# Performance work log

Hardware: AMD Instinct MI355X
Metric: run time of the kernel (lower is better)

Reference implementation:

```python
import jax, jax.numpy as jnp
import numpy as np
import math

N_NODES = 50000
N_EDGES = 1600000
C = 256
H = 8
HD = C // H


def setup_inputs() -> dict:
    key = jax.random.key(0)
    ks = jax.random.split(key, 16)
    s = 0.02
    d = {
        "feat": jax.random.normal(ks[0], (N_NODES, C), jnp.float32),
        "edge_src": jax.random.randint(ks[1], (N_EDGES,), 0, N_NODES),
        "edge_dst": jax.random.randint(ks[2], (N_EDGES,), 0, N_NODES),
        # torch nn.Linear weights are [out, in]
        "Wq": jax.random.normal(ks[3], (C, C), jnp.float32) * s,
        "bq": jnp.zeros((C,), jnp.float32),
        "Wk": jax.random.normal(ks[4], (C, C), jnp.float32) * s,
        "bk": jnp.zeros((C,), jnp.float32),
        "Wv": jax.random.normal(ks[5], (C, C), jnp.float32) * s,
        "bv": jnp.zeros((C,), jnp.float32),
        "Wp": jax.random.normal(ks[6], (C, C), jnp.float32) * s,
        "bp": jnp.zeros((C,), jnp.float32),
        "ln_g": jnp.ones((C,), jnp.float32),
        "ln_b": jnp.zeros((C,), jnp.float32),
        "W1": jax.random.normal(ks[7], (4 * C, C), jnp.float32) * s,
        "b1": jnp.zeros((4 * C,), jnp.float32),
        "W2": jax.random.normal(ks[8], (C, 4 * C), jnp.float32) * s,
        "b2": jnp.zeros((C,), jnp.float32),
    }
    return d


def _layernorm(x, g, b, eps=1e-5):
    mu = jnp.mean(x, axis=-1, keepdims=True)
    var = jnp.mean(jnp.square(x - mu), axis=-1, keepdims=True)
    return (x - mu) * jax.lax.rsqrt(var + eps) * g + b


def reference(feat, edge_src, edge_dst, Wq, bq, Wk, bk, Wv, bv, Wp, bp,
              ln_g, ln_b, W1, b1, W2, b2):
    n = feat.shape[0]
    q = (feat @ Wq.T + bq).reshape(n, H, HD)
    k = (feat @ Wk.T + bk).reshape(n, H, HD)
    v = (feat @ Wv.T + bv).reshape(n, H, HD)

    # per-edge attention logits: (q[dst] * k[src]).sum(-1) / sqrt(head_dim), clamped
    score = jnp.einsum('ehd,ehd->eh', q[edge_dst], k[edge_src])  # [E, H]
    score = jnp.clip(score / math.sqrt(HD), -10.0, 10.0)

    # destination-grouped (segment) softmax over incoming edges
    smax = jax.ops.segment_max(score, edge_dst, num_segments=n)
    smax = jnp.where(jnp.isfinite(smax), smax, 0.0)  # guard empty segments
    ex = jnp.exp(score - smax[edge_dst])
    den = jax.ops.segment_sum(ex, edge_dst, num_segments=n)
    alpha = ex / den[edge_dst]  # [E, H]

    # weighted scatter-aggregate: sum_e alpha_e * v[src_e] into dst
    wv = jax.ops.segment_sum(alpha[:, :, None] * v[edge_src], edge_dst,
                             num_segments=n).reshape(n, C)

    y = wv @ Wp.T + bp
    x = feat + y
    h = _layernorm(x, ln_g, ln_b)
    h = jax.nn.gelu(h @ W1.T + b1, approximate=False) @ W2.T + b2
    return x + h
```

## Files before the change

### kernel.cpp

```cpp
#include <hip/hip_runtime.h>
#include <hip/hip_bf16.h>

#define CDIM 256
#define NH 8
#define HDIM 32

typedef short bf8 __attribute__((ext_vector_type(8)));
typedef float f32x4 __attribute__((ext_vector_type(4)));
typedef float f32x2 __attribute__((ext_vector_type(2)));

__device__ __forceinline__ float bf2f(ushort u) {
  union { unsigned int i; float f; } x; x.i = ((unsigned int)u) << 16; return x.f;
}
__device__ __forceinline__ ushort f2bf(float f) {
  union { float f; unsigned int i; } x; x.f = f;
  unsigned int lsb = (x.i >> 16) & 1u;
  unsigned int r = x.i + 0x7fffu + lsb;
  return (ushort)(r >> 16);
}

__device__ __forceinline__ float dec_e4m3_sw(unsigned int b) {
  unsigned int s = b >> 7, e = (b >> 3) & 15, m = b & 7;
  float v = (e == 0) ? (float)m * 0.001953125f
                     : (float)(8 + m) * 0.125f * exp2f((float)((int)e - 7));
  return s ? -v : v;
}
__device__ __forceinline__ unsigned char enc_e4m3_sw(float f) {
  union { float f; unsigned int u; } x; x.f = f;
  unsigned int s = (x.u >> 31) << 7;
  float a = fabsf(f);
  if (!(a > 0.f)) return (unsigned char)s;
  if (a > 448.f) a = 448.f;
  int e = 0; float mant = frexpf(a, &e);
  int E = e + 6;
  unsigned int out;
  if (E <= 0) {
    int m = (int)rintf(a * 512.f);
    out = (m > 7) ? (s | (1u << 3)) : (s | (unsigned)m);
  } else {
    int m = (int)rintf(mant * 16.f);
    if (m == 16) { m = 8; E++; }
    if (E > 15 || (E == 15 && m - 8 > 6)) { E = 15; m = 14; }
    out = s | ((unsigned)E << 3) | (unsigned)(m - 8);
  }
  return (unsigned char)out;
}
template <bool HI>
__device__ __forceinline__ f32x2 fp8x2_f32(unsigned int w) {
#if __has_builtin(__builtin_amdgcn_cvt_pk_f32_fp8)
  return __builtin_amdgcn_cvt_pk_f32_fp8(w, HI);
#else
  unsigned int b0 = HI ? ((w >> 16) & 0xffu) : (w & 0xffu);
  unsigned int b1 = HI ? (w >> 24) : ((w >> 8) & 0xffu);
  f32x2 r; r[0] = dec_e4m3_sw(b0); r[1] = dec_e4m3_sw(b1); return r;
#endif
}
__device__ __forceinline__ unsigned char f32_fp8(float f) {
#if __has_builtin(__builtin_amdgcn_cvt_pk_fp8_f32)
  return (unsigned char)(__builtin_amdgcn_cvt_pk_fp8_f32(f, f, 0, false) & 0xff);
#else
  return enc_e4m3_sw(f);
#endif
}

__device__ __forceinline__ float fast_gelu(float t) {
  float u = 0.7978845608028654f * (t + 0.044715f * t * t * t);
  float ez = __expf(2.f * u);
  float th = 1.f - 2.f * __builtin_amdgcn_rcpf(ez + 1.f);
  return 0.5f * t * (1.f + th);
}

__device__ __forceinline__ void gload_lds16(const ushort* g, ushort* l) {
  __builtin_amdgcn_global_load_lds((const __attribute__((address_space(1))) unsigned int*)g,
                                   (__attribute__((address_space(3))) unsigned int*)l,
                                   16, 0, 0);
}

__global__ void k_cast4(const float4* __restrict__ s, ushort4* __restrict__ d, int n4) {
  int i = blockIdx.x * blockDim.x + threadIdx.x;
  if (i < n4) {
    float4 v = s[i];
    ushort4 o;
    o.x = f2bf(v.x); o.y = f2bf(v.y); o.z = f2bf(v.z); o.w = f2bf(v.w);
    d[i] = o;
  }
}

__global__ void k_hist(const int* __restrict__ dst, int E, int* __restrict__ deg) {
  int i = blockIdx.x * blockDim.x + threadIdx.x;
  if (i < E) atomicAdd(&deg[dst[i]], 1);
}

__global__ __launch_bounds__(1024) void k_scan1(const int* __restrict__ deg, int N,
                                                int* __restrict__ rowptr, int* __restrict__ bsum) {
  __shared__ int s[1024];
  int t = threadIdx.x;
  int i = blockIdx.x * 1024 + t;
  int val = (i < N) ? deg[i] : 0;
  s[t] = val;
  __syncthreads();
  for (int off = 1; off < 1024; off <<= 1) {
    int add = (t >= off) ? s[t - off] : 0;
    __syncthreads();
    s[t] += add;
    __syncthreads();
  }
  if (i < N) rowptr[i + 1] = s[t];
  if (t == 1023) bsum[blockIdx.x] = s[t];
}

__global__ void k_scan2(int* __restrict__ bsum, int nb) {
  if (threadIdx.x == 0 && blockIdx.x == 0) {
    int run = 0;
    for (int j = 0; j < nb; ++j) { int t = bsum[j]; bsum[j] = run; run += t; }
  }
}

__global__ void k_scan3(int* __restrict__ rowptr, const int* __restrict__ bsum, int N) {
  int i = blockIdx.x * blockDim.x + threadIdx.x;
  if (i < N) rowptr[i + 1] += bsum[i >> 10];
  if (i == 0) rowptr[0] = 0;
}

__global__ void k_scatter(const int* __restrict__ src, const int* __restrict__ dst, int E,
                          const int* __restrict__ rowptr, int* __restrict__ cur,
                          int* __restrict__ csr_src) {
  int i = blockIdx.x * blockDim.x + threadIdx.x;
  if (i < E) {
    int d = dst[i];
    int pos = rowptr[d] + atomicAdd(&cur[d], 1);
    csr_src[pos] = src[i];
  }
}

__device__ __forceinline__ void stage_tile(const ushort* __restrict__ S, int ld,
                                           int r0, int nr, int k0,
                                           ushort* lds, int wave, int lane) {
#pragma unroll
  for (int j = 0; j < 2; ++j) {
    int g = wave * 128 + j * 64 + lane;
    int row = g >> 2, slot = g & 3;
    int rr = r0 + row; rr = (rr < nr) ? rr : (nr - 1);
    const ushort* src = S + (size_t)rr * ld + k0 + ((slot ^ (row & 3)) << 3);
    gload_lds16(src, &lds[(size_t)(wave * 128 + j * 64) * 8]);
  }
}

__device__ __forceinline__ void gemm128_core(const ushort* __restrict__ A, int lda, int rowt, int nA,
                                             const ushort* __restrict__ B, int ldb, int colt, int nB,
                                             int K, ushort* lA, ushort* lB, f32x4* acc) {
  int tid = threadIdx.x;
  int wave = tid >> 6, lane = tid & 63;
  int m = lane & 15, quad = lane >> 4;
  int r0w = (wave & 1) * 64, c0w = (wave >> 1) * 64;
  int sw = (quad ^ (m & 3)) << 3;

  for (int k0 = 0; k0 < K; k0 += 32) {
    __syncthreads();
    stage_tile(A, lda, rowt, nA, k0, lA, wave, lane);
    stage_tile(B, ldb, colt, nB, k0, lB, wave, lane);
    __syncthreads();

    bf8 a[4], b[4];
#pragma unroll
    for (int ri = 0; ri < 4; ++ri)
      a[ri] = *(const bf8*)&lA[(r0w + ri * 16 + m) * 32 + sw];
#pragma unroll
    for (int cj = 0; cj < 4; ++cj)
      b[cj] = *(const bf8*)&lB[(c0w + cj * 16 + m) * 32 + sw];
#pragma unroll
    for (int ri = 0; ri < 4; ++ri)
#pragma unroll
      for (int cj = 0; cj < 4; ++cj)
        acc[ri * 4 + cj] = __builtin_amdgcn_mfma_f32_16x16x32_bf16(a[ri], b[cj], acc[ri * 4 + cj], 0, 0, 0);
  }
}

__global__ __launch_bounds__(256) void k_qkvf(const ushort* __restrict__ featb,
                                              const ushort* __restrict__ Wqkv,
                                              const float* __restrict__ bq, const float* __restrict__ bk,
                                              const float* __restrict__ bv,
                                              ushort* __restrict__ q,
                                              unsigned char* __restrict__ k8,
                                              unsigned char* __restrict__ v8, int N) {
  __shared__ ushort lA[128 * 32];
  __shared__ ushort lB[128 * 32];
  int rowt = blockIdx.x * 128, colt = blockIdx.y * 128;
  int which = colt >> 8;
  const float* bias = (which == 0) ? bq : (which == 1) ? bk : bv;
  int tid = threadIdx.x;
  int wave = tid >> 6, lane = tid & 63, m = lane & 15, quad = lane >> 4;
  int r0w = (wave & 1) * 64, c0w = (wave >> 1) * 64;

  f32x4 acc[16];
#pragma unroll
  for (int j = 0; j < 16; ++j) acc[j] = (f32x4){0.f, 0.f, 0.f, 0.f};

  gemm128_core(featb, CDIM, rowt, N, Wqkv, CDIM, colt, 768, CDIM, lA, lB, acc);

  unsigned char* o8 = (which == 1) ? k8 : v8;
#pragma unroll
  for (int cj = 0; cj < 4; ++cj) {
    int col = (colt + c0w + cj * 16 + m) & 255;
    float bs = bias[col];
#pragma unroll
    for (int ri = 0; ri < 4; ++ri)
#pragma unroll
      for (int i = 0; i < 4; ++i) {
        int r = rowt + r0w + ri * 16 + quad * 4 + i;
        if (r < N) {
          float vv = acc[ri * 4 + cj][i] + bs;
          if (which == 0) q[(size_t)r * CDIM + col] = f2bf(vv);
          else            o8[(size_t)r * CDIM + col] = f32_fp8(vv);
        }
      }
  }
}

__global__ __launch_bounds__(256) void k_proj(const ushort* __restrict__ wv,
                                              const ushort* __restrict__ Wp,
                                              const float* __restrict__ bp,
                                              const float* __restrict__ feat,
                                              float* __restrict__ x, int N) {
  __shared__ ushort lA[128 * 32];
  __shared__ ushort lB[128 * 32];
  int rowt = blockIdx.x * 128, colt = blockIdx.y * 128;
  int tid = threadIdx.x;
  int wave = tid >> 6, lane = tid & 63, m = lane & 15, quad = lane >> 4;
  int r0w = (wave & 1) * 64, c0w = (wave >> 1) * 64;

  f32x4 acc[16];
#pragma unroll
  for (int j = 0; j < 16; ++j) acc[j] = (f32x4){0.f, 0.f, 0.f, 0.f};

  gemm128_core(wv, CDIM, rowt, N, Wp, CDIM, colt, 256, CDIM, lA, lB, acc);

#pragma unroll
  for (int cj = 0; cj < 4; ++cj) {
    int col = colt + c0w + cj * 16 + m;
    float bs = bp[col];
#pragma unroll
    for (int ri = 0; ri < 4; ++ri)
#pragma unroll
      for (int i = 0; i < 4; ++i) {
        int r = rowt + r0w + ri * 16 + quad * 4 + i;
        if (r < N)
          x[(size_t)r * CDIM + col] = acc[ri * 4 + cj][i] + bs + feat[(size_t)r * CDIM + col];
      }
  }
}

__global__ __launch_bounds__(256) void k_g1(const ushort* __restrict__ h,
                                            const ushort* __restrict__ W1c,
                                            const float* __restrict__ b1c,
                                            ushort* __restrict__ hid, int N) {
  __shared__ ushort lA[128 * 32];
  __shared__ ushort lB[128 * 32];
  int rowt = blockIdx.x * 128, colt = blockIdx.y * 128;
  int tid = threadIdx.x;
  int wave = tid >> 6, lane = tid & 63, m = lane & 15, quad = lane >> 4;
  int r0w = (wave & 1) * 64, c0w = (wave >> 1) * 64;

  f32x4 acc[16];
#pragma unroll
  for (int j = 0; j < 16; ++j) acc[j] = (f32x4){0.f, 0.f, 0.f, 0.f};

  gemm128_core(h, CDIM, rowt, N, W1c, CDIM, colt, 512, CDIM, lA, lB, acc);

#pragma unroll
  for (int cj = 0; cj < 4; ++cj) {
    int col = colt + c0w + cj * 16 + m;
    float bs = b1c[col];
#pragma unroll
    for (int ri = 0; ri < 4; ++ri)
#pragma unroll
      for (int i = 0; i < 4; ++i) {
        int r = rowt + r0w + ri * 16 + quad * 4 + i;
        if (r < N) hid[(size_t)r * 512 + col] = f2bf(fast_gelu(acc[ri * 4 + cj][i] + bs));
      }
  }
}

__global__ __launch_bounds__(256) void k_g2(const ushort* __restrict__ hid,
                                            const ushort* __restrict__ W2c,
                                            const float* __restrict__ b2,
                                            float* __restrict__ out, int N, int first) {
  __shared__ ushort lA[128 * 32];
  __shared__ ushort lB[128 * 32];
  int rowt = blockIdx.x * 128, colt = blockIdx.y * 128;
  int tid = threadIdx.x;
  int wave = tid >> 6, lane = tid & 63, m = lane & 15, quad = lane >> 4;
  int r0w = (wave & 1) * 64, c0w = (wave >> 1) * 64;

  f32x4 acc[16];
#pragma unroll
  for (int j = 0; j < 16; ++j) acc[j] = (f32x4){0.f, 0.f, 0.f, 0.f};

  gemm128_core(hid, 512, rowt, N, W2c, 1024, colt, 256, 512, lA, lB, acc);

#pragma unroll
  for (int cj = 0; cj < 4; ++cj) {
    int col = colt + c0w + cj * 16 + m;
    float bs = first ? b2[col] : 0.f;
#pragma unroll
    for (int ri = 0; ri < 4; ++ri)
#pragma unroll
      for (int i = 0; i < 4; ++i) {
        int r = rowt + r0w + ri * 16 + quad * 4 + i;
        if (r < N) {
          size_t idx = (size_t)r * CDIM + col;
          out[idx] = out[idx] + acc[ri * 4 + cj][i] + bs;
        }
      }
  }
}

__global__ __launch_bounds__(256) void k_edge_agg(const ushort* __restrict__ q,
                                                  const unsigned char* __restrict__ kk8,
                                                  const unsigned char* __restrict__ vv8,
                                                  const int* __restrict__ rowptr,
                                                  const int* __restrict__ csr_src,
                                                  int N,
                                                  ushort* __restrict__ wv) {
  int wave = threadIdx.x >> 6, lane = threadIdx.x & 63;
  int n = blockIdx.x * 4 + wave;
  if (n >= N) return;

  int el = lane >> 3, h = lane & 7;
  int beg = rowptr[n], end = rowptr[n + 1];
  int deg = end - beg;

  float qf[32];
  {
    const ushort* qp = q + (size_t)n * CDIM + h * HDIM;
#pragma unroll
    for (int g = 0; g < 4; ++g) {
      bf8 qv = *(const bf8*)(qp + g * 8);
#pragma unroll
      for (int j = 0; j < 8; ++j) qf[g * 8 + j] = bf2f((ushort)qv[j]);
    }
  }

  float accv[4] = {0.f, 0.f, 0.f, 0.f};
  float den_part = 0.f;

  for (int c0 = 0; c0 < deg; c0 += 8) {
    int src = 0;
    float e = 0.f;
    if (c0 + el < deg) {
      src = csr_src[beg + c0 + el];
      const unsigned char* kp = kk8 + (size_t)src * CDIM + h * HDIM;
      uint4 w0 = *(const uint4*)kp;
      uint4 w1 = *(const uint4*)(kp + 16);
      unsigned int ws[8] = {w0.x, w0.y, w0.z, w0.w, w1.x, w1.y, w1.z, w1.w};
      float dot = 0.f;
#pragma unroll
      for (int j = 0; j < 8; ++j) {
        f32x2 lo = fp8x2_f32<false>(ws[j]);
        f32x2 hi = fp8x2_f32<true>(ws[j]);
        dot = fmaf(qf[j * 4 + 0], lo[0], dot);
        dot = fmaf(qf[j * 4 + 1], lo[1], dot);
        dot = fmaf(qf[j * 4 + 2], hi[0], dot);
        dot = fmaf(qf[j * 4 + 3], hi[1], dot);
      }
      float s = dot * 0.17677669529663687f;
      s = fminf(10.f, fmaxf(-10.f, s));
      e = __expf(s - 10.f);
    }
    den_part += e;

#pragma unroll
    for (int j = 0; j < 8; ++j) {
      int sj = __shfl(src, j << 3);
      float ej = __shfl(e, (j << 3) | (lane >> 3));
      unsigned int vw = *(const unsigned int*)(vv8 + (size_t)sj * CDIM + lane * 4);
      f32x2 lo = fp8x2_f32<false>(vw);
      f32x2 hi = fp8x2_f32<true>(vw);
      accv[0] = fmaf(ej, lo[0], accv[0]);
      accv[1] = fmaf(ej, lo[1], accv[1]);
      accv[2] = fmaf(ej, hi[0], accv[2]);
      accv[3] = fmaf(ej, hi[1], accv[3]);
    }
  }

  float den = den_part;
  den += __shfl_xor(den, 8);
  den += __shfl_xor(den, 16);
  den += __shfl_xor(den, 32);
  float denh = __shfl(den, lane >> 3);

  float inv = (deg > 0) ? (1.f / denh) : 0.f;
  ushort4 o;
  o.x = f2bf(accv[0] * inv);
  o.y = f2bf(accv[1] * inv);
  o.z = f2bf(accv[2] * inv);
  o.w = f2bf(accv[3] * inv);
  *(ushort4*)(wv + (size_t)n * CDIM + lane * 4) = o;
}

__global__ __launch_bounds__(256) void k_ln(const float* __restrict__ x,
                                            const float* __restrict__ g,
                                            const float* __restrict__ b,
                                            ushort* __restrict__ h,
                                            float* __restrict__ out) {
  int row = blockIdx.x * 4 + (threadIdx.x >> 6);
  int lane = threadIdx.x & 63;
  const float* xr = x + (size_t)row * CDIM;
  float4 xv = *(const float4*)(xr + lane * 4);
  *(float4*)(out + (size_t)row * CDIM + lane * 4) = xv;
  float s = xv.x + xv.y + xv.z + xv.w;
  float ss = xv.x * xv.x + xv.y * xv.y + xv.z * xv.z + xv.w * xv.w;
#pragma unroll
  for (int msk = 1; msk <= 32; msk <<= 1) {
    s += __shfl_xor(s, msk);
    ss += __shfl_xor(ss, msk);
  }
  float mu = s * (1.f / CDIM);
  float var = ss * (1.f / CDIM) - mu * mu;
  float rs = rsqrtf(var + 1e-5f);
  float xe[4] = {xv.x, xv.y, xv.z, xv.w};
#pragma unroll
  for (int t = 0; t < 4; ++t) {
    int cc = lane * 4 + t;
    h[(size_t)row * CDIM + cc] = f2bf((xe[t] - mu) * rs * g[cc] + b[cc]);
  }
}

extern "C" void kernel_launch(void* const* d_in, const int* in_sizes, int n_in,
                              void* d_out, int out_size, void* d_ws, size_t ws_size,
                              hipStream_t stream) {
  const float* feat = (const float*)d_in[0];
  const int* esrc = (const int*)d_in[1];
  const int* edst = (const int*)d_in[2];
  const float* Wq = (const float*)d_in[3];
  const float* bq = (const float*)d_in[4];
  const float* Wk = (const float*)d_in[5];
  const float* bk = (const float*)d_in[6];
  const float* Wv = (const float*)d_in[7];
  const float* bv = (const float*)d_in[8];
  const float* Wp = (const float*)d_in[9];
  const float* bp = (const float*)d_in[10];
  const float* lng = (const float*)d_in[11];
  const float* lnb = (const float*)d_in[12];
  const float* W1 = (const float*)d_in[13];
  const float* b1 = (const float*)d_in[14];
  const float* W2 = (const float*)d_in[15];
  const float* b2 = (const float*)d_in[16];

  const int N = in_sizes[0] / CDIM;
  const int E = in_sizes[1];
  const size_t NC2 = (size_t)N * CDIM * 2;
  const size_t NC1 = (size_t)N * CDIM;

  char* w = (char*)d_ws;
  ushort* q   = (ushort*)(w);
  unsigned char* k8 = (unsigned char*)(w + NC2);
  unsigned char* v8 = (unsigned char*)(w + NC2 + NC1);
  ushort* wvb = (ushort*)(w + 3 * NC2);
  ushort* featb = (ushort*)(w + 3 * NC2);
  float*  x   = (float*)(w);
  ushort* h   = (ushort*)(w + 2 * NC2);
  ushort* hid = (ushort*)(w);

  char* csr = w + 4 * NC2;
  int* rowptr  = (int*)(csr);
  int* deg     = (int*)(csr + 200064);
  int* csr_src = (int*)(csr + 400128);
  int* bsum    = (int*)(csr + 400128 + (size_t)E * 4);

  char* wb = csr + 400128 + (size_t)E * 4 + 256;
  ushort* Wqb = (ushort*)(wb);
  ushort* Wkb = (ushort*)(wb + 131072);
  ushort* Wvb = (ushort*)(wb + 262144);
  ushort* Wpb = (ushort*)(wb + 393216);
  ushort* W1b = (ushort*)(wb + 524288);
  ushort* W2b = (ushort*)(wb + 1048576);

  const int nb = (N + 1023) / 1024;
  const int RT128 = (N + 127) / 128;

  k_cast4<<<(16384 + 255) / 256, 256, 0, stream>>>((const float4*)Wq, (ushort4*)Wqb, 16384);
  k_cast4<<<(16384 + 255) / 256, 256, 0, stream>>>((const float4*)Wk, (ushort4*)Wkb, 16384);
  k_cast4<<<(16384 + 255) / 256, 256, 0, stream>>>((const float4*)Wv, (ushort4*)Wvb, 16384);
  k_cast4<<<(16384 + 255) / 256, 256, 0, stream>>>((const float4*)Wp, (ushort4*)Wpb, 16384);
  k_cast4<<<(65536 + 255) / 256, 256, 0, stream>>>((const float4*)W1, (ushort4*)W1b, 65536);
  k_cast4<<<(65536 + 255) / 256, 256, 0, stream>>>((const float4*)W2, (ushort4*)W2b, 65536);
  {
    int n4 = N * CDIM / 4;
    k_cast4<<<(n4 + 255) / 256, 256, 0, stream>>>((const float4*)feat, (ushort4*)featb, n4);
  }

  hipMemsetAsync(deg, 0, (size_t)N * 4, stream);
  k_hist<<<(E + 255) / 256, 256, 0, stream>>>(edst, E, deg);
  k_scan1<<<nb, 1024, 0, stream>>>(deg, N, rowptr, bsum);
  k_scan2<<<1, 64, 0, stream>>>(bsum, nb);
  k_scan3<<<(N + 255) / 256, 256, 0, stream>>>(rowptr, bsum, N);
  hipMemsetAsync(deg, 0, (size_t)N * 4, stream);
  k_scatter<<<(E + 255) / 256, 256, 0, stream>>>(esrc, edst, E, rowptr, deg, csr_src);

  k_qkvf<<<dim3(RT128, 6), 256, 0, stream>>>(featb, Wqb, bq, bk, bv, q, k8, v8, N);
  k_edge_agg<<<(N + 3) / 4, 256, 0, stream>>>(q, k8, v8, rowptr, csr_src, N, wvb);
  k_proj<<<dim3(RT128, 2), 256, 0, stream>>>(wvb, Wpb, bp, feat, x, N);
  k_ln<<<N / 4, 256, 0, stream>>>(x, lng, lnb, h, (float*)d_out);

  for (int c = 0; c < 2; ++c) {
    k_g1<<<dim3(RT128, 4), 256, 0, stream>>>(h, W1b + (size_t)c * 512 * CDIM,
                                             b1 + c * 512, hid, N);
    k_g2<<<dim3(RT128, 2), 256, 0, stream>>>(hid, W2b + (size_t)c * 512,
                                             b2, (float*)d_out, N, c == 0 ? 1 : 0);
  }
}
```

Baseline: 780.6 us.

## Widen GEMM tiles to 128x256 with 8 waves and prefetch edge keys

All four GEMM kernels now launch 512-thread blocks covering a 128x256 output tile. The A tile is staged once per 8 waves and reused across twice as many columns, which halves the grid and cuts redundant A loads. Separately, the edge aggregation loop software-pipelines the next chunk's csr_src index and fp8 key loads ahead of the current dot products to hide gather latency. The larger blocks use more LDS per block and may reduce occupancy, and the prefetch adds register pressure plus one extra load past the last chunk.

Result: faster. 720.8 us (-7.7%).

```diff
diff --git a/kernel.cpp b/kernel.cpp
--- a/kernel.cpp
+++ b/kernel.cpp
@@ -133,9 +133,19 @@
   }
 }
 
-__device__ __forceinline__ void stage_tile(const ushort* __restrict__ S, int ld,
-                                           int r0, int nr, int k0,
-                                           ushort* lds, int wave, int lane) {
+__device__ __forceinline__ void stageA8(const ushort* __restrict__ S, int ld,
+                                        int r0, int nr, int k0,
+                                        ushort* lds, int wave, int lane) {
+  int g = wave * 64 + lane;
+  int row = g >> 2, slot = g & 3;
+  int rr = r0 + row; rr = (rr < nr) ? rr : (nr - 1);
+  const ushort* src = S + (size_t)rr * ld + k0 + ((slot ^ (row & 3)) << 3);
+  gload_lds16(src, &lds[(size_t)(wave * 64) * 8]);
+}
+
+__device__ __forceinline__ void stageB8(const ushort* __restrict__ S, int ld,
+                                        int r0, int nr, int k0,
+                                        ushort* lds, int wave, int lane) {
 #pragma unroll
   for (int j = 0; j < 2; ++j) {
     int g = wave * 128 + j * 64 + lane;
@@ -146,7 +156,7 @@
   }
 }
 
-__device__ __forceinline__ void gemm128_core(const ushort* __restrict__ A, int lda, int rowt, int nA,
+__device__ __forceinline__ void gemm256_core(const ushort* __restrict__ A, int lda, int rowt, int nA,
                                              const ushort* __restrict__ B, int ldb, int colt, int nB,
                                              int K, ushort* lA, ushort* lB, f32x4* acc) {
   int tid = threadIdx.x;
@@ -157,8 +167,8 @@
 
   for (int k0 = 0; k0 < K; k0 += 32) {
     __syncthreads();
-    stage_tile(A, lda, rowt, nA, k0, lA, wave, lane);
-    stage_tile(B, ldb, colt, nB, k0, lB, wave, lane);
+    stageA8(A, lda, rowt, nA, k0, lA, wave, lane);
+    stageB8(B, ldb, colt, nB, k0, lB, wave, lane);
     __syncthreads();
 
     bf8 a[4], b[4];
@@ -176,7 +186,7 @@
   }
 }
 
-__global__ __launch_bounds__(256) void k_qkvf(const ushort* __restrict__ featb,
+__global__ __launch_bounds__(512) void k_qkvf(const ushort* __restrict__ featb,
                                               const ushort* __restrict__ Wqkv,
                                               const float* __restrict__ bq, const float* __restrict__ bk,
                                               const float* __restrict__ bv,
@@ -184,9 +194,9 @@
                                               unsigned char* __restrict__ k8,
                                               unsigned char* __restrict__ v8, int N) {
   __shared__ ushort lA[128 * 32];
-  __shared__ ushort lB[128 * 32];
-  int rowt = blockIdx.x * 128, colt = blockIdx.y * 128;
-  int which = colt >> 8;
+  __shared__ ushort lB[256 * 32];
+  int rowt = blockIdx.x * 128;
+  int which = blockIdx.y;
   const float* bias = (which == 0) ? bq : (which == 1) ? bk : bv;
   int tid = threadIdx.x;
   int wave = tid >> 6, lane = tid & 63, m = lane & 15, quad = lane >> 4;
@@ -196,12 +206,13 @@
 #pragma unroll
   for (int j = 0; j < 16; ++j) acc[j] = (f32x4){0.f, 0.f, 0.f, 0.f};
 
-  gemm128_core(featb, CDIM, rowt, N, Wqkv, CDIM, colt, 768, CDIM, lA, lB, acc);
+  gemm256_core(featb, CDIM, rowt, N, Wqkv + (size_t)which * 256 * CDIM, CDIM, 0, 256,
+               CDIM, lA, lB, acc);
 
   unsigned char* o8 = (which == 1) ? k8 : v8;
 #pragma unroll
   for (int cj = 0; cj < 4; ++cj) {
-    int col = (colt + c0w + cj * 16 + m) & 255;
+    int col = c0w + cj * 16 + m;
     float bs = bias[col];
 #pragma unroll
     for (int ri = 0; ri < 4; ++ri)
@@ -217,14 +228,14 @@
   }
 }
 
-__global__ __launch_bounds__(256) void k_proj(const ushort* __restrict__ wv,
+__global__ __launch_bounds__(512) void k_proj(const ushort* __restrict__ wv,
                                               const ushort* __restrict__ Wp,
                                               const float* __restrict__ bp,
                                               const float* __restrict__ feat,
                                               float* __restrict__ x, int N) {
   __shared__ ushort lA[128 * 32];
-  __shared__ ushort lB[128 * 32];
-  int rowt = blockIdx.x * 128, colt = blockIdx.y * 128;
+  __shared__ ushort lB[256 * 32];
+  int rowt = blockIdx.x * 128;
   int tid = threadIdx.x;
   int wave = tid >> 6, lane = tid & 63, m = lane & 15, quad = lane >> 4;
   int r0w = (wave & 1) * 64, c0w = (wave >> 1) * 64;
@@ -233,11 +244,11 @@
 #pragma unroll
   for (int j = 0; j < 16; ++j) acc[j] = (f32x4){0.f, 0.f, 0.f, 0.f};
 
-  gemm128_core(wv, CDIM, rowt, N, Wp, CDIM, colt, 256, CDIM, lA, lB, acc);
+  gemm256_core(wv, CDIM, rowt, N, Wp, CDIM, 0, 256, CDIM, lA, lB, acc);
 
 #pragma unroll
   for (int cj = 0; cj < 4; ++cj) {
-    int col = colt + c0w + cj * 16 + m;
+    int col = c0w + cj * 16 + m;
     float bs = bp[col];
 #pragma unroll
     for (int ri = 0; ri < 4; ++ri)
@@ -250,13 +261,13 @@
   }
 }
 
-__global__ __launch_bounds__(256) void k_g1(const ushort* __restrict__ h,
+__global__ __launch_bounds__(512) void k_g1(const ushort* __restrict__ h,
                                             const ushort* __restrict__ W1c,
                                             const float* __restrict__ b1c,
                                             ushort* __restrict__ hid, int N) {
   __shared__ ushort lA[128 * 32];
-  __shared__ ushort lB[128 * 32];
-  int rowt = blockIdx.x * 128, colt = blockIdx.y * 128;
+  __shared__ ushort lB[256 * 32];
+  int rowt = blockIdx.x * 128, colt = blockIdx.y * 256;
   int tid = threadIdx.x;
   int wave = tid >> 6, lane = tid & 63, m = lane & 15, quad = lane >> 4;
   int r0w = (wave & 1) * 64, c0w = (wave >> 1) * 64;
@@ -265,7 +276,7 @@
 #pragma unroll
   for (int j = 0; j < 16; ++j) acc[j] = (f32x4){0.f, 0.f, 0.f, 0.f};
 
-  gemm128_core(h, CDIM, rowt, N, W1c, CDIM, colt, 512, CDIM, lA, lB, acc);
+  gemm256_core(h, CDIM, rowt, N, W1c, CDIM, colt, 512, CDIM, lA, lB, acc);
 
 #pragma unroll
   for (int cj = 0; cj < 4; ++cj) {
@@ -281,13 +292,13 @@
   }
 }
 
-__global__ __launch_bounds__(256) void k_g2(const ushort* __restrict__ hid,
+__global__ __launch_bounds__(512) void k_g2(const ushort* __restrict__ hid,
                                             const ushort* __restrict__ W2c,
                                             const float* __restrict__ b2,
                                             float* __restrict__ out, int N, int first) {
   __shared__ ushort lA[128 * 32];
-  __shared__ ushort lB[128 * 32];
-  int rowt = blockIdx.x * 128, colt = blockIdx.y * 128;
+  __shared__ ushort lB[256 * 32];
+  int rowt = blockIdx.x * 128;
   int tid = threadIdx.x;
   int wave = tid >> 6, lane = tid & 63, m = lane & 15, quad = lane >> 4;
   int r0w = (wave & 1) * 64, c0w = (wave >> 1) * 64;
@@ -296,11 +307,11 @@
 #pragma unroll
   for (int j = 0; j < 16; ++j) acc[j] = (f32x4){0.f, 0.f, 0.f, 0.f};
 
-  gemm128_core(hid, 512, rowt, N, W2c, 1024, colt, 256, 512, lA, lB, acc);
+  gemm256_core(hid, 512, rowt, N, W2c, 1024, 0, 256, 512, lA, lB, acc);
 
 #pragma unroll
   for (int cj = 0; cj < 4; ++cj) {
-    int col = colt + c0w + cj * 16 + m;
+    int col = c0w + cj * 16 + m;
     float bs = first ? b2[col] : 0.f;
 #pragma unroll
     for (int ri = 0; ri < 4; ++ri)
@@ -344,14 +355,23 @@
   float accv[4] = {0.f, 0.f, 0.f, 0.f};
   float den_part = 0.f;
 
+  int src_n = (el < deg) ? csr_src[beg + el] : 0;
+  const unsigned char* kp0 = kk8 + (size_t)src_n * CDIM + h * HDIM;
+  uint4 w0_n = *(const uint4*)kp0;
+  uint4 w1_n = *(const uint4*)(kp0 + 16);
+
   for (int c0 = 0; c0 < deg; c0 += 8) {
-    int src = 0;
+    int src = src_n;
+    uint4 w0 = w0_n, w1 = w1_n;
+    bool vcur = (c0 + el < deg);
+
+    src_n = (c0 + 8 + el < deg) ? csr_src[beg + c0 + 8 + el] : 0;
+    const unsigned char* kpn = kk8 + (size_t)src_n * CDIM + h * HDIM;
+    w0_n = *(const uint4*)kpn;
+    w1_n = *(const uint4*)(kpn + 16);
+
     float e = 0.f;
-    if (c0 + el < deg) {
-      src = csr_src[beg + c0 + el];
-      const unsigned char* kp = kk8 + (size_t)src * CDIM + h * HDIM;
-      uint4 w0 = *(const uint4*)kp;
-      uint4 w1 = *(const uint4*)(kp + 16);
+    if (vcur) {
       unsigned int ws[8] = {w0.x, w0.y, w0.z, w0.w, w1.x, w1.y, w1.z, w1.w};
       float dot = 0.f;
 #pragma unroll
@@ -498,15 +518,15 @@
   hipMemsetAsync(deg, 0, (size_t)N * 4, stream);
   k_scatter<<<(E + 255) / 256, 256, 0, stream>>>(esrc, edst, E, rowptr, deg, csr_src);
 
-  k_qkvf<<<dim3(RT128, 6), 256, 0, stream>>>(featb, Wqb, bq, bk, bv, q, k8, v8, N);
+  k_qkvf<<<dim3(RT128, 3), 512, 0, stream>>>(featb, Wqb, bq, bk, bv, q, k8, v8, N);
   k_edge_agg<<<(N + 3) / 4, 256, 0, stream>>>(q, k8, v8, rowptr, csr_src, N, wvb);
-  k_proj<<<dim3(RT128, 2), 256, 0, stream>>>(wvb, Wpb, bp, feat, x, N);
+  k_proj<<<RT128, 512, 0, stream>>>(wvb, Wpb, bp, feat, x, N);
   k_ln<<<N / 4, 256, 0, stream>>>(x, lng, lnb, h, (float*)d_out);
 
   for (int c = 0; c < 2; ++c) {
-    k_g1<<<dim3(RT128, 4), 256, 0, stream>>>(h, W1b + (size_t)c * 512 * CDIM,
+    k_g1<<<dim3(RT128, 2), 512, 0, stream>>>(h, W1b + (size_t)c * 512 * CDIM,
                                              b1 + c * 512, hid, N);
-    k_g2<<<dim3(RT128, 2), 256, 0, stream>>>(hid, W2b + (size_t)c * 512,
-                                             b2, (float*)d_out, N, c == 0 ? 1 : 0);
-  }
-}
+    k_g2<<<RT128, 512, 0, stream>>>(hid, W2b + (size_t)c * 512,
+                                    b2, (float*)d_out, N, c == 0 ? 1 : 0);
+  }
+}
```
